# Optimization experiments

Measured on AMD Instinct MI355X. Metric: run time of the kernel, lower is better.

The kernel has to match this reference:

```python
import jax, jax.numpy as jnp
from jax import lax
import numpy as np

B, T, C = 2048, 512, 32  # batch, max_seq_len, num_tags


def setup_inputs() -> dict:
    key = jax.random.key(0)
    k1, k2, k3, k4 = jax.random.split(key, 4)
    logits = jax.random.normal(k1, (B, T, C), dtype=jnp.float32)
    sequence_length = jax.random.randint(k2, (B,), 1, T + 1, dtype=jnp.int32)
    labels = jax.random.randint(k3, (B, T), 0, C, dtype=jnp.int32)
    # learned CRF transition matrix (orthogonal init approximated by normal)
    transitions = jax.random.normal(k4, (C, C), dtype=jnp.float32)
    return dict(logits=logits, sequence_length=sequence_length,
                labels=labels, transitions=transitions)


def _viterbi_decode(logits, transitions, seq_len):
    """tfa_text.crf_decode: returns highest-scoring tag sequence [B, T] int32."""
    Bn, Tn, Cn = logits.shape
    identity_bp = jnp.arange(Cn, dtype=jnp.int32)[None, :]  # carries tag through padding

    def fwd(state, xs):  # state: [B, C] viterbi scores
        logit_t, t = xs
        scores = state[:, :, None] + transitions[None]       # [B, C_prev, C_cur]
        cand = logit_t + jnp.max(scores, axis=1)             # [B, C]
        bp = jnp.argmax(scores, axis=1).astype(jnp.int32)    # [B, C] best prev tag
        active = (t < seq_len)[:, None]
        return (jnp.where(active, cand, state),
                jnp.where(active, bp, identity_bp))

    xs = (jnp.swapaxes(logits[:, 1:], 0, 1), jnp.arange(1, Tn))
    final_state, bps = lax.scan(fwd, logits[:, 0], xs)       # bps: [T-1, B, C]
    last_tag = jnp.argmax(final_state, axis=-1).astype(jnp.int32)  # [B]

    def back(tag, bp):  # tag at t+1 -> tag at t
        prev = jnp.take_along_axis(bp, tag[:, None], axis=1)[:, 0]
        return prev, tag

    first_tag, later_tags = lax.scan(back, last_tag, bps, reverse=True)
    tags = jnp.concatenate([first_tag[None], later_tags], axis=0).T  # [B, T]
    valid = jnp.arange(Tn)[None, :] < seq_len[:, None]
    return jnp.where(valid, tags, 0)


def _crf_log_likelihood(logits, labels, transitions, seq_len):
    """tfa_text.crf_log_likelihood: per-example log-likelihood [B]."""
    Bn, Tn, Cn = logits.shape

    # --- log partition via forward algorithm ---
    def fwd(alpha, xs):
        logit_t, t = xs
        new = jax.nn.logsumexp(alpha[:, :, None] + transitions[None], axis=1) + logit_t
        active = (t < seq_len)[:, None]
        return jnp.where(active, new, alpha), None

    xs = (jnp.swapaxes(logits[:, 1:], 0, 1), jnp.arange(1, Tn))
    alpha, _ = lax.scan(fwd, logits[:, 0], xs)
    log_norm = jax.nn.logsumexp(alpha, axis=-1)  # [B]

    # --- score of gold label sequence ---
    pos = jnp.arange(Tn)
    mask = (pos[None, :] < seq_len[:, None]).astype(logits.dtype)          # [B, T]
    unary = jnp.sum(
        jnp.take_along_axis(logits, labels[..., None], axis=2)[..., 0] * mask,
        axis=1)
    pair_mask = (pos[None, :-1] < (seq_len - 1)[:, None]).astype(logits.dtype)
    binary = jnp.sum(transitions[labels[:, :-1], labels[:, 1:]] * pair_mask, axis=1)

    return unary + binary - log_norm


def reference(logits, sequence_length, labels, transitions):
    # training=True path: labels clamped to >= 0 (already non-negative here)
    labels = jnp.maximum(labels, 0)
    decode_tags = _viterbi_decode(logits, transitions, sequence_length)
    log_likelihood = _crf_log_likelihood(logits, labels, transitions, sequence_length)
    loss = jnp.mean(-log_likelihood)  # recorded via add_loss in the original
    return decode_tags, loss
```

## Files before the change

### kernel.cpp

```cpp
#include <hip/hip_runtime.h>
#include <math.h>

#define BB 2048
#define TT 512
#define CC 32

#if __has_builtin(__builtin_amdgcn_exp2f)
#define EXP2F __builtin_amdgcn_exp2f
#else
#define EXP2F exp2f
#endif
#if __has_builtin(__builtin_amdgcn_logf)
#define LOG2F __builtin_amdgcn_logf
#else
#define LOG2F log2f
#endif

#define LOG2E 1.4426950408889634f
#define LN2   0.6931471805599453f

__global__ void zero_loss_kernel(float* __restrict__ out) {
  if (threadIdx.x == 0) out[(size_t)BB * TT] = 0.0f;
}

__global__ void schedule_kernel(const int* __restrict__ seqlen,
                                int* __restrict__ perm,
                                float* __restrict__ out) {
  __shared__ int s[TT];
  __shared__ int off[TT];
  const int tid = threadIdx.x;
  if (tid == 0) out[(size_t)BB * TT] = 0.0f;
  s[tid] = 0;
  __syncthreads();
  for (int b = tid; b < BB; b += TT) atomicAdd(&s[seqlen[b] - 1], 1);
  __syncthreads();
  for (int d = 1; d < TT; d <<= 1) {
    int v = s[tid] + ((tid + d < TT) ? s[tid + d] : 0);
    __syncthreads();
    s[tid] = v;
    __syncthreads();
  }
  off[tid] = (tid + 1 < TT) ? s[tid + 1] : 0;
  __syncthreads();
  for (int b = tid; b < BB; b += TT) {
    int pos = atomicAdd(&off[seqlen[b] - 1], 1);
    perm[pos] = b;
  }
}

#define ROR(dst, src, K)                                                     \
  dst = __int_as_float(__builtin_amdgcn_update_dpp(                          \
      0, __float_as_int(src), 0x120 | (K), 0xF, 0xF, false));

__device__ __forceinline__ float xor16f(float x, int lane) {
#if __has_builtin(__builtin_amdgcn_permlane16_swap)
  auto r = __builtin_amdgcn_permlane16_swap(__float_as_uint(x),
                                            __float_as_uint(x), false, false);
  return __uint_as_float((lane & 16) ? r[0] : r[1]);
#else
  return __int_as_float(
      __builtin_amdgcn_ds_swizzle(__float_as_int(x), 0x401F));
#endif
}
__device__ __forceinline__ float xor32f(float x, int lane) {
#if __has_builtin(__builtin_amdgcn_permlane32_swap)
  auto r = __builtin_amdgcn_permlane32_swap(__float_as_uint(x),
                                            __float_as_uint(x), false, false);
  return __uint_as_float((lane & 32) ? r[0] : r[1]);
#else
  return __shfl_xor(x, 32);
#endif
}
__device__ __forceinline__ int xor32i(int x, int lane) {
#if __has_builtin(__builtin_amdgcn_permlane32_swap)
  auto r = __builtin_amdgcn_permlane32_swap((unsigned)x, (unsigned)x,
                                            false, false);
  return (int)((lane & 32) ? r[0] : r[1]);
#else
  return __shfl_xor(x, 32);
#endif
}

__global__ __launch_bounds__(128, 4) void crf_kernel(
    const float* __restrict__ logits,
    const int*   __restrict__ seqlen,
    const int*   __restrict__ labels,
    const float* __restrict__ trans,
    float*       __restrict__ out,
    const int*   __restrict__ perm)
{
  __shared__ __align__(16) unsigned char bp_s[(TT - 1) * CC];
  __shared__ unsigned char tag_s[TT];

  const int lane = threadIdx.x & 63;
  const int wv   = threadIdx.x >> 6;
  const int k    = blockIdx.x;

  const int bs0 = perm ? perm[k] : k;
  const int bs1 = perm ? perm[BB - 1 - k] : -1;

  const int i  = lane & 15;
  const int c  = lane & 31;
  const int r  = (lane >> 4) & 1;
  const int pr = (lane < 32) ? r : 1 - r;

  if (wv == 0) {
    float tr2[16];
    int   pidx[16];
#pragma unroll
    for (int kk = 0; kk < 16; ++kk) {
      int p = pr * 16 + ((i - kk) & 15);
      pidx[kk] = p;
      tr2[kk] = trans[p * CC + c];
    }

    for (int sq = 0; sq < 2; ++sq) {
      const int b = sq ? bs1 : bs0;
      if (b < 0) break;
      const int len = seqlen[b];
      const float* lg = logits + (size_t)b * TT * CC;
      const size_t bT = (size_t)b * TT;

      float av = lg[c];

      const float* lgc = lg + c;
      float l0 = 0, l1 = 0, l2 = 0;
      {
        int r1 = 1 < len ? 1 : len - 1;
        int r2 = 2 < len ? 2 : len - 1;
        int r3 = 3 < len ? 3 : len - 1;
        l0 = lgc[r1 * CC]; l1 = lgc[r2 * CC]; l2 = lgc[r3 * CC];
      }

      auto vstep = [&](int t, float logit_c) {
        float base = (lane < 32) ? av : xor16f(av, lane);
        float S[16];
        float x;
        S[0] = base + tr2[0];
        ROR(x, base, 1);  S[1]  = x + tr2[1];
        ROR(x, base, 2);  S[2]  = x + tr2[2];
        ROR(x, base, 3);  S[3]  = x + tr2[3];
        ROR(x, base, 4);  S[4]  = x + tr2[4];
        ROR(x, base, 5);  S[5]  = x + tr2[5];
        ROR(x, base, 6);  S[6]  = x + tr2[6];
        ROR(x, base, 7);  S[7]  = x + tr2[7];
        ROR(x, base, 8);  S[8]  = x + tr2[8];
        ROR(x, base, 9);  S[9]  = x + tr2[9];
        ROR(x, base, 10); S[10] = x + tr2[10];
        ROR(x, base, 11); S[11] = x + tr2[11];
        ROR(x, base, 12); S[12] = x + tr2[12];
        ROR(x, base, 13); S[13] = x + tr2[13];
        ROR(x, base, 14); S[14] = x + tr2[14];
        ROR(x, base, 15); S[15] = x + tr2[15];

        float m8[8];
#pragma unroll
        for (int kk = 0; kk < 8; ++kk) m8[kk] = fmaxf(S[kk], S[kk + 8]);
#pragma unroll
        for (int kk = 0; kk < 4; ++kk) m8[kk] = fmaxf(m8[kk], m8[kk + 4]);
        float best = fmaxf(fmaxf(m8[0], m8[2]), fmaxf(m8[1], m8[3]));

        int t8[16];
#pragma unroll
        for (int kk = 0; kk < 16; ++kk)
          t8[kk] = (S[kk] == best) ? pidx[kk] : 63;
#pragma unroll
        for (int kk = 0; kk < 8; ++kk) t8[kk] = min(t8[kk], t8[kk + 8]);
#pragma unroll
        for (int kk = 0; kk < 4; ++kk) t8[kk] = min(t8[kk], t8[kk + 4]);
        int bi = min(min(t8[0], t8[2]), min(t8[1], t8[3]));

        float ov = xor32f(best, lane);
        int   oi = xor32i(bi, lane);
        bool take = (ov > best) || (ov == best && oi < bi);
        best = take ? ov : best;
        int bpi = take ? oi : bi;
        av = logit_c + best;

        if (lane < 32) bp_s[(t - 1) * CC + c] = (unsigned char)bpi;
      };

      int t = 1;
      int tmain = len - 3;
      for (; t < tmain; ++t) {
        float lc = l0; l0 = l1; l1 = l2;
        l2 = lgc[(t + 3) * CC];
        vstep(t, lc);
      }
      for (; t < len; ++t) {
        float lc = l0; l0 = l1; l1 = l2;
        int rn = t + 3; rn = rn < len ? rn : len - 1;
        l2 = lgc[rn * CC];
        vstep(t, lc);
      }

      float v = av; int idx = c;
#pragma unroll
      for (int d = 1; d < 32; d <<= 1) {
        float v2 = __shfl_xor(v, d, 32);
        int   i2 = __shfl_xor(idx, d, 32);
        if (v2 > v || (v2 == v && i2 < idx)) { v = v2; idx = i2; }
      }

      if (lane == 0) {
        int tag = idx;
        tag_s[len - 1] = (unsigned char)tag;
        const uint4* bp4 = (const uint4*)bp_s;
        uint4 Ra[3], Rb[3];
#pragma unroll
        for (int kk = 0; kk < 3; ++kk) {
          int rr = len - 2 - kk;
          if (rr >= 0) { Ra[kk] = bp4[2 * rr]; Rb[kk] = bp4[2 * rr + 1]; }
        }
        for (int tt = len - 1; tt > 0; --tt) {
          uint4 ua = Ra[0], ub = Rb[0];
          Ra[0] = Ra[1]; Rb[0] = Rb[1];
          Ra[1] = Ra[2]; Rb[1] = Rb[2];
          int rr = tt - 4;
          if (rr >= 0) { Ra[2] = bp4[2 * rr]; Rb[2] = bp4[2 * rr + 1]; }
          uint4 u4;
          u4.x = (tag & 16) ? ub.x : ua.x;
          u4.y = (tag & 16) ? ub.y : ua.y;
          u4.z = (tag & 16) ? ub.z : ua.z;
          u4.w = (tag & 16) ? ub.w : ua.w;
          unsigned lo = (tag & 8) ? u4.z : u4.x;
          unsigned hi = (tag & 8) ? u4.w : u4.y;
          unsigned u1 = (tag & 4) ? hi : lo;
          tag = (int)((u1 >> ((tag & 3) * 8)) & 0xffu);
          tag_s[tt - 1] = (unsigned char)tag;
        }
      }

#pragma unroll
      for (int j = 0; j < 8; ++j) {
        int tt = lane + 64 * j;
        float val = (tt < len) ? (float)tag_s[tt] : 0.0f;
        out[bT + tt] = val;
      }
    }

  } else {
    float E[16];
#pragma unroll
    for (int kk = 0; kk < 16; ++kk) {
      int p = pr * 16 + ((i - kk) & 15);
      E[kk] = EXP2F(trans[p * CC + c] * LOG2E);
    }

    float loss_acc = 0.0f;

    for (int sq = 0; sq < 2; ++sq) {
      const int b = sq ? bs1 : bs0;
      if (b < 0) break;
      const int len = seqlen[b];
      const float* lg = logits + (size_t)b * TT * CC;
      const int* lab = labels + (size_t)b * TT;

      float P   = EXP2F(lg[c] * LOG2E);
      float Acc = 0.0f;

      const float* lgc = lg + c;
      float e0 = 0, e1 = 0, e2 = 0;
      {
        int r1 = 1 < len ? 1 : len - 1;
        int r2 = 2 < len ? 2 : len - 1;
        int r3 = 3 < len ? 3 : len - 1;
        e0 = EXP2F(lgc[r1 * CC] * LOG2E);
        e1 = EXP2F(lgc[r2 * CC] * LOG2E);
        e2 = EXP2F(lgc[r3 * CC] * LOG2E);
      }

      auto fstep = [&](float el) {
        float base = (lane < 32) ? P : xor16f(P, lane);
        float x;
        float a0 = base * E[0];
        ROR(x, base, 1);  float a1 = x * E[1];
        ROR(x, base, 2);  float a2 = x * E[2];
        ROR(x, base, 3);  float a3 = x * E[3];
        ROR(x, base, 4);  a0 = fmaf(x, E[4],  a0);
        ROR(x, base, 5);  a1 = fmaf(x, E[5],  a1);
        ROR(x, base, 6);  a2 = fmaf(x, E[6],  a2);
        ROR(x, base, 7);  a3 = fmaf(x, E[7],  a3);
        ROR(x, base, 8);  a0 = fmaf(x, E[8],  a0);
        ROR(x, base, 9);  a1 = fmaf(x, E[9],  a1);
        ROR(x, base, 10); a2 = fmaf(x, E[10], a2);
        ROR(x, base, 11); a3 = fmaf(x, E[11], a3);
        ROR(x, base, 12); a0 = fmaf(x, E[12], a0);
        ROR(x, base, 13); a1 = fmaf(x, E[13], a1);
        ROR(x, base, 14); a2 = fmaf(x, E[14], a2);
        ROR(x, base, 15); a3 = fmaf(x, E[15], a3);
        float part = (a0 + a1) + (a2 + a3);
        float oth  = xor32f(part, lane);
        P = el * (part + oth);
      };

      auto renorm = [&]() {
        float m = P, y;
        ROR(y, m, 8); m = fmaxf(m, y);
        ROR(y, m, 4); m = fmaxf(m, y);
        ROR(y, m, 2); m = fmaxf(m, y);
        ROR(y, m, 1); m = fmaxf(m, y);
        m = fmaxf(m, xor16f(m, lane));
        int e = (int)(__float_as_uint(m) >> 23) - 127;
        P = ldexpf(P, -e);
        Acc += (float)e;
      };

      int t = 1;
      int tmain = len - 3;
      for (; t < tmain; ++t) {
        float ec = e0; e0 = e1; e1 = e2;
        e2 = EXP2F(lgc[(t + 3) * CC] * LOG2E);
        fstep(ec);
        if ((t & 3) == 0) renorm();
      }
      for (; t < len; ++t) {
        float ec = e0; e0 = e1; e1 = e2;
        int rn = t + 3; rn = rn < len ? rn : len - 1;
        e2 = EXP2F(lgc[rn * CC] * LOG2E);
        fstep(ec);
        if ((t & 3) == 0) renorm();
      }

      float uacc = 0.0f, bacc = 0.0f;
#pragma unroll
      for (int j = 0; j < 8; ++j) {
        int tt = lane + 64 * j;
        if (tt < len) {
          int lt = lab[tt];
          uacc += lg[tt * CC + lt];
          if (tt + 1 < len) {
            int ln = lab[tt + 1];
            bacc += trans[lt * CC + ln];
          }
        }
      }
#pragma unroll
      for (int d = 32; d >= 1; d >>= 1) {
        uacc += __shfl_xor(uacc, d);
        bacc += __shfl_xor(bacc, d);
      }

      float ss = P, y2;
      ROR(y2, ss, 8); ss += y2;
      ROR(y2, ss, 4); ss += y2;
      ROR(y2, ss, 2); ss += y2;
      ROR(y2, ss, 1); ss += y2;
      ss += xor16f(ss, lane);
      float log_norm = LN2 * (Acc + LOG2F(ss));

      loss_acc += (uacc + bacc - log_norm);
    }

    if (lane == 0) {
      atomicAdd(out + (size_t)BB * TT, loss_acc * (-1.0f / BB));
    }
  }
}

extern "C" void kernel_launch(void* const* d_in, const int* in_sizes, int n_in,
                              void* d_out, int out_size, void* d_ws, size_t ws_size,
                              hipStream_t stream) {
  const float* logits = (const float*)d_in[0];
  const int*   seqlen = (const int*)d_in[1];
  const int*   labels = (const int*)d_in[2];
  const float* trans  = (const float*)d_in[3];
  float* out = (float*)d_out;

  if (d_ws != nullptr && ws_size >= BB * sizeof(int)) {
    int* perm = (int*)d_ws;
    schedule_kernel<<<1, TT, 0, stream>>>(seqlen, perm, out);
    crf_kernel<<<dim3(BB / 2), dim3(128), 0, stream>>>(
        logits, seqlen, labels, trans, out, perm);
  } else {
    zero_loss_kernel<<<1, 64, 0, stream>>>(out);
    crf_kernel<<<dim3(BB), dim3(128), 0, stream>>>(
        logits, seqlen, labels, trans, out, nullptr);
  }
}
```

Baseline: 429.7 us.

## Double-buffer logit loads in 8-step blocks for Viterbi and forward recursions

Replaces the 3-deep rolling prefetch of per-step logits in both the Viterbi and forward-algorithm loops with two 8-element register buffers. One block of loads is issued while the other block's steps run, so the serial recurrence has more global-load latency hidden. The exp of the logit moves into the forward step. The backtrace loop also gets an unroll-4 pragma. This adds register pressure and per-step bounds checks inside the unrolled blocks.

```diff
diff --git a/kernel.cpp b/kernel.cpp
--- a/kernel.cpp
+++ b/kernel.cpp
@@ -120,17 +120,9 @@
       const int len = seqlen[b];
       const float* lg = logits + (size_t)b * TT * CC;
       const size_t bT = (size_t)b * TT;
+      const float* lgc = lg + c;
 
       float av = lg[c];
-
-      const float* lgc = lg + c;
-      float l0 = 0, l1 = 0, l2 = 0;
-      {
-        int r1 = 1 < len ? 1 : len - 1;
-        int r2 = 2 < len ? 2 : len - 1;
-        int r3 = 3 < len ? 3 : len - 1;
-        l0 = lgc[r1 * CC]; l1 = lgc[r2 * CC]; l2 = lgc[r3 * CC];
-      }
 
       auto vstep = [&](int t, float logit_c) {
         float base = (lane < 32) ? av : xor16f(av, lane);
@@ -180,18 +172,29 @@
         if (lane < 32) bp_s[(t - 1) * CC + c] = (unsigned char)bpi;
       };
 
-      int t = 1;
-      int tmain = len - 3;
-      for (; t < tmain; ++t) {
-        float lc = l0; l0 = l1; l1 = l2;
-        l2 = lgc[(t + 3) * CC];
-        vstep(t, lc);
-      }
-      for (; t < len; ++t) {
-        float lc = l0; l0 = l1; l1 = l2;
-        int rn = t + 3; rn = rn < len ? rn : len - 1;
-        l2 = lgc[rn * CC];
-        vstep(t, lc);
+      float Abk[8], Bbk[8];
+      auto loadB = [&](float (&bk)[8], int t0) {
+#pragma unroll
+        for (int s = 0; s < 8; ++s) {
+          int tt = t0 + s; tt = tt < len ? tt : len - 1;
+          bk[s] = lgc[tt * CC];
+        }
+      };
+      auto runB = [&](float (&bk)[8], int t0) {
+#pragma unroll
+        for (int s = 0; s < 8; ++s) {
+          int tt = t0 + s;
+          if (tt < len) vstep(tt, bk[s]);
+        }
+      };
+      loadB(Abk, 1);
+      for (int t0 = 1; t0 < len; t0 += 16) {
+        loadB(Bbk, t0 + 8);
+        runB(Abk, t0);
+        if (t0 + 8 < len) {
+          loadB(Abk, t0 + 16);
+          runB(Bbk, t0 + 8);
+        }
       }
 
       float v = av; int idx = c;
@@ -212,6 +215,7 @@
           int rr = len - 2 - kk;
           if (rr >= 0) { Ra[kk] = bp4[2 * rr]; Rb[kk] = bp4[2 * rr + 1]; }
         }
+#pragma unroll 4
         for (int tt = len - 1; tt > 0; --tt) {
           uint4 ua = Ra[0], ub = Rb[0];
           Ra[0] = Ra[1]; Rb[0] = Rb[1];
@@ -255,22 +259,13 @@
       const int len = seqlen[b];
       const float* lg = logits + (size_t)b * TT * CC;
       const int* lab = labels + (size_t)b * TT;
+      const float* lgc = lg + c;
 
       float P   = EXP2F(lg[c] * LOG2E);
       float Acc = 0.0f;
 
-      const float* lgc = lg + c;
-      float e0 = 0, e1 = 0, e2 = 0;
-      {
-        int r1 = 1 < len ? 1 : len - 1;
-        int r2 = 2 < len ? 2 : len - 1;
-        int r3 = 3 < len ? 3 : len - 1;
-        e0 = EXP2F(lgc[r1 * CC] * LOG2E);
-        e1 = EXP2F(lgc[r2 * CC] * LOG2E);
-        e2 = EXP2F(lgc[r3 * CC] * LOG2E);
-      }
-
-      auto fstep = [&](float el) {
+      auto fstep = [&](float raw_logit) {
+        float el = EXP2F(raw_logit * LOG2E);
         float base = (lane < 32) ? P : xor16f(P, lane);
         float x;
         float a0 = base * E[0];
@@ -306,20 +301,32 @@
         Acc += (float)e;
       };
 
-      int t = 1;
-      int tmain = len - 3;
-      for (; t < tmain; ++t) {
-        float ec = e0; e0 = e1; e1 = e2;
-        e2 = EXP2F(lgc[(t + 3) * CC] * LOG2E);
-        fstep(ec);
-        if ((t & 3) == 0) renorm();
-      }
-      for (; t < len; ++t) {
-        float ec = e0; e0 = e1; e1 = e2;
-        int rn = t + 3; rn = rn < len ? rn : len - 1;
-        e2 = EXP2F(lgc[rn * CC] * LOG2E);
-        fstep(ec);
-        if ((t & 3) == 0) renorm();
+      float Abk[8], Bbk[8];
+      auto loadB = [&](float (&bk)[8], int t0) {
+#pragma unroll
+        for (int s = 0; s < 8; ++s) {
+          int tt = t0 + s; tt = tt < len ? tt : len - 1;
+          bk[s] = lgc[tt * CC];
+        }
+      };
+      auto runB = [&](float (&bk)[8], int t0) {
+#pragma unroll
+        for (int s = 0; s < 8; ++s) {
+          int tt = t0 + s;
+          if (tt < len) {
+            fstep(bk[s]);
+            if ((tt & 3) == 0) renorm();
+          }
+        }
+      };
+      loadB(Abk, 1);
+      for (int t0 = 1; t0 < len; t0 += 16) {
+        loadB(Bbk, t0 + 8);
+        runB(Abk, t0);
+        if (t0 + 8 < len) {
+          loadB(Abk, t0 + 16);
+          runB(Bbk, t0 + 8);
+        }
       }
 
       float uacc = 0.0f, bacc = 0.0f;
```

Result: faster. 409.7 us (-4.6%).
